# Kernel tuning notes

Hardware: AMD Instinct MI355X
Metric: run time of the kernel (lower is better)

The kernel has to match this reference:

```python
import jax, jax.numpy as jnp
import numpy as np

N_Q = 5000
MEM = 50
KDIM = 50
VDIM = 200
FC = 50
B = 2048
S = 200


def setup_inputs() -> dict:
    key = jax.random.key(0)
    ks = jax.random.split(key, 14)
    inp = {}
    inp["q_data"] = jax.random.randint(ks[0], (B, S), 0, N_Q, dtype=jnp.int64)
    inp["qa_data"] = jax.random.randint(ks[1], (B, S), 0, 2 * N_Q, dtype=jnp.int64)
    # learned parameters (kaiming-ish random init)
    inp["q_embed_w"] = jax.random.normal(ks[2], (N_Q + 1, KDIM), jnp.float32) * 0.2
    inp["qa_embed_w"] = jax.random.normal(ks[3], (2 * N_Q + 1, VDIM), jnp.float32) * 0.1
    inp["key_memory"] = jax.random.normal(ks[4], (MEM, KDIM), jnp.float32) * 0.2
    inp["init_value_memory"] = jax.random.normal(ks[5], (MEM, VDIM), jnp.float32) * 0.1
    # DKVMN write gates: erase (sigmoid) and add (tanh) transforms of qa embedding
    inp["erase_w"] = jax.random.normal(ks[6], (VDIM, VDIM), jnp.float32) * 0.1
    inp["erase_b"] = jnp.zeros((VDIM,), jnp.float32)
    inp["add_w"] = jax.random.normal(ks[7], (VDIM, VDIM), jnp.float32) * 0.1
    inp["add_b"] = jnp.zeros((VDIM,), jnp.float32)
    # prediction MLP: Linear(VDIM+KDIM -> FC), Tanh, Linear(FC -> 1)
    inp["pred_w1"] = jax.random.normal(ks[8], (VDIM + KDIM, FC), jnp.float32) * 0.1
    inp["pred_b1"] = jnp.zeros((FC,), jnp.float32)
    inp["pred_w2"] = jax.random.normal(ks[9], (FC, 1), jnp.float32) * 0.2
    inp["pred_b2"] = jnp.zeros((1,), jnp.float32)
    return inp


def _dkvmn_forward(q_data, qa_data, q_embed_w, qa_embed_w, key_memory,
                   init_value_memory, erase_w, erase_b, add_w, add_b,
                   pred_w1, pred_b1, pred_w2, pred_b2):
    q_emb = q_embed_w[q_data]    # [B, S, KDIM]
    qa_emb = qa_embed_w[qa_data]  # [B, S, VDIM]
    batch = q_data.shape[0]
    Mv0 = jnp.broadcast_to(init_value_memory, (batch, MEM, VDIM))

    def step(Mv, xs):
        q_t, qa_t = xs  # [B, KDIM], [B, VDIM]
        # attention over memory slots
        w = jax.nn.softmax(q_t @ key_memory.T, axis=-1)          # [B, MEM]
        read = jnp.einsum('bm,bmv->bv', w, Mv)                    # [B, VDIM]
        h = jnp.tanh(jnp.concatenate([read, q_t], -1) @ pred_w1 + pred_b1)
        p = jax.nn.sigmoid((h @ pred_w2 + pred_b2)[:, 0])         # [B]
        # erase/add write
        e = jax.nn.sigmoid(qa_t @ erase_w + erase_b)              # [B, VDIM]
        a = jnp.tanh(qa_t @ add_w + add_b)                        # [B, VDIM]
        Mv_new = Mv * (1.0 - w[:, :, None] * e[:, None, :]) + w[:, :, None] * a[:, None, :]
        return Mv_new, p

    xs = (jnp.swapaxes(q_emb, 0, 1), jnp.swapaxes(qa_emb, 0, 1))  # time-major
    _, preds = jax.lax.scan(step, Mv0, xs)                        # [S, B]
    return preds.T                                                # [B, S]


def reference(q_data, qa_data, q_embed_w, qa_embed_w, key_memory,
              init_value_memory, erase_w, erase_b, add_w, add_b,
              pred_w1, pred_b1, pred_w2, pred_b2):
    preds = _dkvmn_forward(q_data, qa_data, q_embed_w, qa_embed_w, key_memory,
                           init_value_memory, erase_w, erase_b, add_w, add_b,
                           pred_w1, pred_b1, pred_w2, pred_b2)
    zeros = jnp.zeros_like(preds)
    return (preds, zeros, zeros, zeros)
```

## Files before the change

kernel.cpp:

```cpp
#include <hip/hip_runtime.h>
#include <hip/hip_fp16.h>


#define NQ1   5001
#define NQA   10001
#define MEMN  50
#define KD    50
#define VD    200
#define FC    50
#define BB    2048
#define SS    200
#define EA_R  16
#define WHS   32

#define EA_B   626
#define WQ_B   1251
#define PACK_B 8
#define PREP_G (EA_B + WQ_B + PACK_B)

typedef unsigned int   u32;
typedef unsigned short u16;
typedef short    s8v __attribute__((ext_vector_type(8)));
typedef float    f4v __attribute__((ext_vector_type(4)));
typedef _Float16 h2v __attribute__((ext_vector_type(2)));
typedef u32      u4v __attribute__((ext_vector_type(4)));

__device__ __forceinline__ float fast_sigmoid(float x) { return 1.f / (1.f + __expf(-x)); }
__device__ __forceinline__ float fast_tanh(float x) {
    float e2 = __expf(2.f * x);
    return 1.f - 2.f / (e2 + 1.f);
}
__device__ __forceinline__ float bfu16_to_f(u16 u) {
    union { float f; u32 i; } x; x.i = ((u32)u) << 16; return x.f;
}
__device__ __forceinline__ u16 f_to_bfu16(float f) {
    union { float f; u32 i; } x; x.f = f;
    return (u16)((x.i + 0x7fffu + ((x.i >> 16) & 1u)) >> 16);
}
__device__ __forceinline__ h2v u32_to_h2v(u32 u) {
    union { u32 i; h2v h; } x; x.i = u; return x.h;
}
__device__ __forceinline__ u16 f16bits(float f) {
    union { __half h; u16 u; } x; x.h = __float2half(f); return x.u;
}
__device__ __forceinline__ float h16_to_f(u16 u) {
    union { u16 u; __half h; } x; x.u = u; return __half2float(x.h);
}

__global__ __launch_bounds__(256) void prep(
        const float* __restrict__ qemb, const float* __restrict__ km,
        const float* __restrict__ w1,   const float* __restrict__ b1,
        const float* __restrict__ qaemb,
        const float* __restrict__ ew,   const float* __restrict__ ebias,
        const float* __restrict__ aw,   const float* __restrict__ abias,
        float* __restrict__ Wt, u32* __restrict__ Wh, float* __restrict__ Q1,
        u32* __restrict__ EA, u16* __restrict__ W1s,
        float* __restrict__ out_aux) {
    const int tid = threadIdx.x;
    const int blk = blockIdx.x;

    for (size_t i = (size_t)blk * 256 + tid; i < 3ull * BB * SS;
         i += (size_t)PREP_G * 256)
        out_aux[i] = 0.f;

    __shared__ float smem[VD * EA_R];

    if (blk < EA_B) {
        const int r0 = blk * EA_R;
        if (tid < VD) {
            #pragma unroll
            for (int r = 0; r < EA_R; ++r) {
                int row = r0 + r;
                smem[tid * EA_R + r] = (row < NQA) ? qaemb[(size_t)row * VD + tid] : 0.f;
            }
        }
        __syncthreads();
        if (tid >= VD) return;

        float accE[EA_R], accA[EA_R];
        #pragma unroll
        for (int r = 0; r < EA_R; ++r) { accE[r] = 0.f; accA[r] = 0.f; }
        for (int k = 0; k < VD; ++k) {
            float we = ew[k * VD + tid];
            float wa = aw[k * VD + tid];
            #pragma unroll
            for (int r = 0; r < EA_R; ++r) {
                float qv = smem[k * EA_R + r];
                accE[r] = fmaf(qv, we, accE[r]);
                accA[r] = fmaf(qv, wa, accA[r]);
            }
        }
        float be = ebias[tid], ba = abias[tid];
        #pragma unroll
        for (int r = 0; r < EA_R; ++r) {
            int row = r0 + r;
            if (row < NQA) {
                u16 ne16 = f16bits(-fast_sigmoid(accE[r] + be));
                u16 a16  = f16bits(fast_tanh(accA[r] + ba));
                EA[(size_t)row * VD + tid] = (u32)ne16 | ((u32)a16 << 16);
            }
        }
    } else if (blk < EA_B + WQ_B) {
        const int lane = tid & 63;
        const int wv   = tid >> 6;
        const int q    = (blk - EA_B) * 4 + wv;
        const bool qok = q < NQ1;
        float* qrow = smem + wv * 64;
        if (qok && lane < KD) qrow[lane] = qemb[q * KD + lane];
        __syncthreads();
        if (!qok) return;

        float s = -1e30f;
        if (lane < MEMN) {
            s = 0.f;
            #pragma unroll
            for (int k = 0; k < KD; ++k) s = fmaf(qrow[k], km[lane * KD + k], s);
        }
        float mx = s;
        #pragma unroll
        for (int off = 32; off >= 1; off >>= 1) mx = fmaxf(mx, __shfl_xor(mx, off, 64));
        float e = (lane < MEMN) ? __expf(s - mx) : 0.f;
        float sum = e;
        #pragma unroll
        for (int off = 32; off >= 1; off >>= 1) sum += __shfl_xor(sum, off, 64);
        float wv_ = (lane < MEMN) ? (e / sum) : 0.f;
        if (lane < MEMN) Wt[q * MEMN + lane] = wv_;

        float plo = __shfl(wv_, 2 * (lane & 31), 64);
        float phi = __shfl(wv_, 2 * (lane & 31) + 1, 64);
        if (lane < 25) {
            Wh[q * WHS + lane] = (u32)f16bits(plo) | ((u32)f16bits(phi) << 16);
        } else if (lane < WHS) {
            Wh[q * WHS + lane] = 0;
        }

        if (lane < FC) {
            float h = b1[lane];
            #pragma unroll
            for (int k = 0; k < KD; ++k)
                h = fmaf(qrow[k], w1[(VD + k) * FC + lane], h);
            Q1[q * FC + lane] = h;
        }
    } else {
        for (int idx = (blk - EA_B - WQ_B) * 256 + tid; idx < 4 * 7 * 64 * 8;
             idx += PACK_B * 256) {
            int j    = idx & 7;
            int lane = (idx >> 3) & 63;
            int kt   = (idx >> 9) % 7;
            int nt   = idx / 3584;
            int k = kt * 32 + ((lane >> 4) << 3) + j;
            int n = nt * 16 + (lane & 15);
            float v = (k < VD && n < FC) ? w1[k * FC + n] : 0.f;
            W1s[idx] = f_to_bfu16(v);
        }
    }
}

__device__ __forceinline__ void state_step(const u32 (&w)[25], u32 ea,
                                           h2v (&mv)[25], float& rdA, float& rdB) {
    h2v nev2 = u32_to_h2v(__builtin_amdgcn_perm(ea, ea, 0x01000100u));
    h2v av2  = u32_to_h2v(__builtin_amdgcn_perm(ea, ea, 0x03020302u));
    rdA = 0.f; rdB = 0.f;
    #pragma unroll
    for (int i = 0; i < 25; i += 2) {
        h2v w0 = u32_to_h2v(w[i]);
#if __has_builtin(__builtin_amdgcn_fdot2)
        rdA = __builtin_amdgcn_fdot2(w0, mv[i], rdA, false);
#else
        rdA = fmaf((float)w0.x, (float)mv[i].x,
              fmaf((float)w0.y, (float)mv[i].y, rdA));
#endif
        mv[i] = __builtin_elementwise_fma(
            w0, __builtin_elementwise_fma(nev2, mv[i], av2), mv[i]);
        if (i + 1 < 25) {
            h2v w1p = u32_to_h2v(w[i + 1]);
#if __has_builtin(__builtin_amdgcn_fdot2)
            rdB = __builtin_amdgcn_fdot2(w1p, mv[i + 1], rdB, false);
#else
            rdB = fmaf((float)w1p.x, (float)mv[i + 1].x,
                  fmaf((float)w1p.y, (float)mv[i + 1].y, rdB));
#endif
            mv[i + 1] = __builtin_elementwise_fma(
                w1p, __builtin_elementwise_fma(nev2, mv[i + 1], av2), mv[i + 1]);
        }
    }
}

__global__ __launch_bounds__(128) void dkvmn_state(
        const int* __restrict__ qd, const int* __restrict__ qad,
        const u32* __restrict__ Wh, const u32* __restrict__ EA,
        const float* __restrict__ ivm, u16* __restrict__ READ) {
    const int tid  = threadIdx.x;
    const int lane = tid & 63;
    const int wid  = tid >> 6;
    const int blk  = blockIdx.x;
    const int b    = blk >> 1;
    const int role = (blk & 1) * 2 + wid;
    const int base = b * SS;

    if (role < 3) {
        const int v = role * 64 + lane;

        h2v mv[25];
        #pragma unroll
        for (int i = 0; i < 25; ++i) {
            mv[i].x = (_Float16)ivm[(2 * i) * VD + v];
            mv[i].y = (_Float16)ivm[(2 * i + 1) * VD + v];
        }

        int q_c = __builtin_amdgcn_readfirstlane(qd[base]);
        int q_n = __builtin_amdgcn_readfirstlane(qd[base + 1]);
        int qa0 = __builtin_amdgcn_readfirstlane(qad[base]);
        int qa1 = __builtin_amdgcn_readfirstlane(qad[base + 1]);
        u32 ea_c = EA[(size_t)qa0 * VD + v];
        u32 ea_n = EA[(size_t)qa1 * VD + v];

        u32 wb0[25], wb1[25];
        #pragma unroll
        for (int i = 0; i < 25; ++i) wb0[i] = Wh[(size_t)q_c * WHS + i];

        for (int t = 0; t < SS; t += 2) {
            {
                #pragma unroll
                for (int i = 0; i < 25; ++i) wb1[i] = Wh[(size_t)q_n * WHS + i];

                int tn = t + 2; tn = (tn < SS) ? tn : (SS - 1);
                int q_nn  = __builtin_amdgcn_readfirstlane(qd[base + tn]);
                int qa_nn = __builtin_amdgcn_readfirstlane(qad[base + tn]);
                u32 ea_nn = EA[(size_t)qa_nn * VD + v];

                float rdA, rdB;
                state_step(wb0, ea_c, mv, rdA, rdB);
                READ[(size_t)(base + t) * VD + v] = f_to_bfu16(rdA + rdB);
                q_c = q_n; q_n = q_nn; ea_c = ea_n; ea_n = ea_nn;
            }
            {
                #pragma unroll
                for (int i = 0; i < 25; ++i) wb0[i] = Wh[(size_t)q_n * WHS + i];

                int tn = t + 3; tn = (tn < SS) ? tn : (SS - 1);
                int q_nn  = __builtin_amdgcn_readfirstlane(qd[base + tn]);
                int qa_nn = __builtin_amdgcn_readfirstlane(qad[base + tn]);
                u32 ea_nn = EA[(size_t)qa_nn * VD + v];

                float rdA, rdB;
                state_step(wb1, ea_c, mv, rdA, rdB);
                READ[(size_t)(base + t + 1) * VD + v] = f_to_bfu16(rdA + rdB);
                q_c = q_n; q_n = q_nn; ea_c = ea_n; ea_n = ea_nn;
            }
        }
    } else {
        const int v8  = lane & 7;
        const int grp = lane >> 3;
        const int v   = 192 + v8;

        h2v mv4[4];
        #pragma unroll
        for (int j = 0; j < 4; ++j) {
            int p = grp * 4 + j;
            if (p < 25) {
                mv4[j].x = (_Float16)ivm[(2 * p) * VD + v];
                mv4[j].y = (_Float16)ivm[(2 * p + 1) * VD + v];
            } else {
                mv4[j].x = (_Float16)0.f;
                mv4[j].y = (_Float16)0.f;
            }
        }

        int q_c = __builtin_amdgcn_readfirstlane(qd[base]);
        int q_n = __builtin_amdgcn_readfirstlane(qd[base + 1]);
        int qa0 = __builtin_amdgcn_readfirstlane(qad[base]);
        int qa1 = __builtin_amdgcn_readfirstlane(qad[base + 1]);
        u32 ea_c = EA[(size_t)qa0 * VD + v];
        u32 ea_n = EA[(size_t)qa1 * VD + v];
        u4v wq_c = *(const u4v*)(Wh + (size_t)q_c * WHS + grp * 4);
        u4v wq_n = *(const u4v*)(Wh + (size_t)q_n * WHS + grp * 4);

        for (int t = 0; t < SS; ++t) {
            int tn = t + 2; tn = (tn < SS) ? tn : (SS - 1);
            int q_nn  = __builtin_amdgcn_readfirstlane(qd[base + tn]);
            int qa_nn = __builtin_amdgcn_readfirstlane(qad[base + tn]);
            u32 ea_nn = EA[(size_t)qa_nn * VD + v];
            u4v wq_nn = *(const u4v*)(Wh + (size_t)q_nn * WHS + grp * 4);

            h2v nev2 = u32_to_h2v(__builtin_amdgcn_perm(ea_c, ea_c, 0x01000100u));
            h2v av2  = u32_to_h2v(__builtin_amdgcn_perm(ea_c, ea_c, 0x03020302u));

            float rd = 0.f;
            #pragma unroll
            for (int j = 0; j < 4; ++j) {
                h2v w2 = u32_to_h2v(wq_c[j]);
#if __has_builtin(__builtin_amdgcn_fdot2)
                rd = __builtin_amdgcn_fdot2(w2, mv4[j], rd, false);
#else
                rd = fmaf((float)w2.x, (float)mv4[j].x,
                     fmaf((float)w2.y, (float)mv4[j].y, rd));
#endif
                mv4[j] = __builtin_elementwise_fma(
                    w2, __builtin_elementwise_fma(nev2, mv4[j], av2), mv4[j]);
            }
            rd += __shfl_xor(rd, 8, 64);
            rd += __shfl_xor(rd, 16, 64);
            rd += __shfl_xor(rd, 32, 64);
            if (grp == 0)
                READ[(size_t)(base + t) * VD + v] = f_to_bfu16(rd);

            q_c = q_n; q_n = q_nn; ea_c = ea_n; ea_n = ea_nn;
            wq_c = wq_n; wq_n = wq_nn;
        }
    }
}

__global__ __launch_bounds__(256) void mlp_pred(
        const u16* __restrict__ RD, const int* __restrict__ qd,
        const float* __restrict__ Q1tab, const u16* __restrict__ W1s,
        const float* __restrict__ w2, const float* __restrict__ b2,
        float* __restrict__ out) {
    const int tid  = threadIdx.x;
    const int lane = tid & 63;
    const int wv   = tid >> 6;
    const int strip = blockIdx.x * 4 + wv;
    const int row0  = strip * 16;

    const int mrow = lane & 15;
    const int quad = lane >> 4;

    s8v a[7];
    {
        const u16* arow = RD + (size_t)(row0 + mrow) * VD + quad * 8;
        #pragma unroll
        for (int kt = 0; kt < 7; ++kt)
            a[kt] = *(const s8v*)(arow + kt * 32);
    }

    const float b2f = b2[0];
    float pf[4] = {0.f, 0.f, 0.f, 0.f};

    #pragma unroll
    for (int nt = 0; nt < 4; ++nt) {
        s8v bfr[7];
        #pragma unroll
        for (int kt = 0; kt < 7; ++kt)
            bfr[kt] = *(const s8v*)(W1s + (((nt * 7 + kt) * 64) + lane) * 8);

        f4v acc = {0.f, 0.f, 0.f, 0.f};
        #pragma unroll
        for (int kt = 0; kt < 7; ++kt)
            acc = __builtin_amdgcn_mfma_f32_16x16x32_bf16(a[kt], bfr[kt], acc, 0, 0, 0);

        const int f = nt * 16 + mrow;
        const float w2f = (f < FC) ? w2[f] : 0.f;
        #pragma unroll
        for (int r = 0; r < 4; ++r) {
            int row = row0 + quad * 4 + r;
            float h = acc[r] + Q1tab[qd[row] * FC + f];
            pf[r] = fmaf(fast_tanh(h), w2f, pf[r]);
        }
    }

    #pragma unroll
    for (int r = 0; r < 4; ++r) {
        float s = pf[r];
        s += __shfl_xor(s, 1, 64);
        s += __shfl_xor(s, 2, 64);
        s += __shfl_xor(s, 4, 64);
        s += __shfl_xor(s, 8, 64);
        if (mrow == 0)
            out[row0 + quad * 4 + r] = fast_sigmoid(s + b2f);
    }
}

__global__ void dkvmn_main(const int* __restrict__ qd, const int* __restrict__ qad,
                           const float* __restrict__ Wtab, const float* __restrict__ Q1tab,
                           const u32* __restrict__ EA,
                           const float* __restrict__ ivm,
                           const float* __restrict__ w1,
                           const float* __restrict__ w2,
                           const float* __restrict__ b2,
                           float* __restrict__ out) {
    const int tid  = threadIdx.x;
    const int b    = blockIdx.x;
    const int v    = tid;
    const int lane = tid & 63;
    const int wv   = tid >> 6;

    __shared__ alignas(16) float read_lds[4 * 52];
    __shared__ alignas(16) float part_lds[4 * 52];

    float mv[MEMN];
    if (v < VD) {
        #pragma unroll
        for (int m = 0; m < MEMN; ++m) mv[m] = ivm[m * VD + v];
    }
    float w1r[50];
    if (lane < FC) {
        #pragma unroll
        for (int i = 0; i < 50; ++i) w1r[i] = w1[(wv * 50 + i) * FC + lane];
    } else {
        #pragma unroll
        for (int i = 0; i < 50; ++i) w1r[i] = 0.f;
    }
    const float w2f = (tid < FC) ? w2[tid] : 0.f;
    const float b2f = b2[0];

    const int* qrow_i  = qd  + b * SS;
    const int* qarow_i = qad + b * SS;
    const int jchunk = v / 50;
    const int wslot  = jchunk * 52 + (v - jchunk * 50);

    for (int t = 0; t < SS; ++t) {
        const int q  = __builtin_amdgcn_readfirstlane(qrow_i[t]);
        const int qa = __builtin_amdgcn_readfirstlane(qarow_i[t]);
        const float* wrow = Wtab + q * MEMN;

        u32 ea = 0;
        if (v < VD) ea = EA[(size_t)qa * VD + v];
        float ne = h16_to_f((u16)(ea & 0xffffu));
        float av = h16_to_f((u16)(ea >> 16));

        if (v < VD) {
            float rd0 = 0.f, rd1 = 0.f;
            #pragma unroll
            for (int m = 0; m < MEMN; m += 2) {
                float wm0 = wrow[m], wm1 = wrow[m + 1];
                rd0 = fmaf(wm0, mv[m], rd0);
                mv[m] = fmaf(wm0, fmaf(ne, mv[m], av), mv[m]);
                rd1 = fmaf(wm1, mv[m + 1], rd1);
                mv[m + 1] = fmaf(wm1, fmaf(ne, mv[m + 1], av), mv[m + 1]);
            }
            read_lds[wslot] = rd0 + rd1;
        }
        __syncthreads();

        float part = 0.f;
        {
            const float* rlc = read_lds + wv * 52;
            #pragma unroll
            for (int i = 0; i < 48; i += 4) {
                float4 x = *(const float4*)(rlc + i);
                part = fmaf(x.x, w1r[i],     part);
                part = fmaf(x.y, w1r[i + 1], part);
                part = fmaf(x.z, w1r[i + 2], part);
                part = fmaf(x.w, w1r[i + 3], part);
            }
            part = fmaf(rlc[48], w1r[48], part);
            part = fmaf(rlc[49], w1r[49], part);
        }
        if (lane < FC) part_lds[wv * 52 + lane] = part;
        __syncthreads();

        if (wv == 0) {
            float pf = 0.f;
            if (lane < FC) {
                float h = part_lds[lane] + part_lds[52 + lane] +
                          part_lds[104 + lane] + part_lds[156 + lane] +
                          Q1tab[q * FC + lane];
                pf = fast_tanh(h) * w2f;
            }
            #pragma unroll
            for (int off = 32; off >= 1; off >>= 1) pf += __shfl_xor(pf, off, 64);
            if (lane == 0) out[b * SS + t] = fast_sigmoid(pf + b2f);
        }
    }
}

extern "C" void kernel_launch(void* const* d_in, const int* in_sizes, int n_in,
                              void* d_out, int out_size, void* d_ws, size_t ws_size,
                              hipStream_t stream) {
    const int* qd  = (const int*)d_in[0];
    const int* qad = (const int*)d_in[1];
    const float* qemb  = (const float*)d_in[2];
    const float* qaemb = (const float*)d_in[3];
    const float* km    = (const float*)d_in[4];
    const float* ivm   = (const float*)d_in[5];
    const float* ew    = (const float*)d_in[6];
    const float* eb    = (const float*)d_in[7];
    const float* aw    = (const float*)d_in[8];
    const float* ab    = (const float*)d_in[9];
    const float* w1    = (const float*)d_in[10];
    const float* b1    = (const float*)d_in[11];
    const float* w2    = (const float*)d_in[12];
    const float* b2    = (const float*)d_in[13];
    float* out = (float*)d_out;
    (void)in_sizes; (void)n_in; (void)out_size;

    char* ws = (char*)d_ws;
    float* Wt  = (float*)(ws);
    float* Q1  = (float*)(ws + 1000448);
    u32*   EA  = (u32*)  (ws + 2000896);
    u16*   W1s = (u16*)  (ws + 10001920);
    u32*   Wh  = (u32*)  (ws + 10034688);
    u16*   RD  = (u16*)  (ws + 10675200);
    const size_t need = 10675200ull + 163840000ull + 512ull;

    prep<<<PREP_G, 256, 0, stream>>>(qemb, km, w1, b1, qaemb, ew, eb, aw, ab,
                                     Wt, Wh, Q1, EA, W1s, out + (size_t)BB * SS);

    if (ws_size >= need) {
        dkvmn_state<<<BB * 2, 128, 0, stream>>>(qd, qad, Wh, EA, ivm, RD);
        mlp_pred<<<(BB * SS) / 64, 256, 0, stream>>>(RD, qd, Q1, W1s, w2, b2, out);
    } else {
        dkvmn_main<<<BB, 256, 0, stream>>>(qd, qad, Wt, Q1, EA, ivm, w1, w2, b2, out);
    }
}
```

Measured before the change: 434.0 us.

## Stage question indices in LDS and load Wh rows as vector VGPR loads

The per-sequence q and qa indices are copied once into shared memory, so each step reads them from LDS instead of issuing scalar global loads. The 25-word attention row is now fetched with six 16-byte vector loads plus one word per lane, where before it was 25 uniform scalar loads. The loop is no longer manually unrolled into two halves with a double-buffered register array. Instead it prefetches indices three steps ahead and the next Wh row one step ahead. This is meant to cut scalar-memory latency and register pressure in the serial recurrence, at the cost of per-lane vector loads of uniform data and an LDS fill with a block barrier.

```diff
diff --git a/kernel.cpp b/kernel.cpp
--- a/kernel.cpp
+++ b/kernel.cpp
@@ -156,14 +156,15 @@
     }
 }
 
-__device__ __forceinline__ void state_step(const u32 (&w)[25], u32 ea,
-                                           h2v (&mv)[25], float& rdA, float& rdB) {
+__device__ __forceinline__ void state_step_v(const u4v (&w)[6], u32 w6, u32 ea,
+                                             h2v (&mv)[25], float& rdA, float& rdB) {
     h2v nev2 = u32_to_h2v(__builtin_amdgcn_perm(ea, ea, 0x01000100u));
     h2v av2  = u32_to_h2v(__builtin_amdgcn_perm(ea, ea, 0x03020302u));
     rdA = 0.f; rdB = 0.f;
     #pragma unroll
     for (int i = 0; i < 25; i += 2) {
-        h2v w0 = u32_to_h2v(w[i]);
+        u32 wu0 = (i < 24) ? w[i >> 2][i & 3] : w6;
+        h2v w0 = u32_to_h2v(wu0);
 #if __has_builtin(__builtin_amdgcn_fdot2)
         rdA = __builtin_amdgcn_fdot2(w0, mv[i], rdA, false);
 #else
@@ -173,7 +174,7 @@
         mv[i] = __builtin_elementwise_fma(
             w0, __builtin_elementwise_fma(nev2, mv[i], av2), mv[i]);
         if (i + 1 < 25) {
-            h2v w1p = u32_to_h2v(w[i + 1]);
+            h2v w1p = u32_to_h2v(w[(i + 1) >> 2][(i + 1) & 3]);
 #if __has_builtin(__builtin_amdgcn_fdot2)
             rdB = __builtin_amdgcn_fdot2(w1p, mv[i + 1], rdB, false);
 #else
@@ -198,6 +199,13 @@
     const int role = (blk & 1) * 2 + wid;
     const int base = b * SS;
 
+    __shared__ int qs[SS], qas[SS];
+    for (int i = tid; i < SS; i += 128) {
+        qs[i]  = qd[base + i];
+        qas[i] = qad[base + i];
+    }
+    __syncthreads();
+
     if (role < 3) {
         const int v = role * 64 + lane;
 
@@ -208,46 +216,41 @@
             mv[i].y = (_Float16)ivm[(2 * i + 1) * VD + v];
         }
 
-        int q_c = __builtin_amdgcn_readfirstlane(qd[base]);
-        int q_n = __builtin_amdgcn_readfirstlane(qd[base + 1]);
-        int qa0 = __builtin_amdgcn_readfirstlane(qad[base]);
-        int qa1 = __builtin_amdgcn_readfirstlane(qad[base + 1]);
-        u32 ea_c = EA[(size_t)qa0 * VD + v];
-        u32 ea_n = EA[(size_t)qa1 * VD + v];
-
-        u32 wb0[25], wb1[25];
-        #pragma unroll
-        for (int i = 0; i < 25; ++i) wb0[i] = Wh[(size_t)q_c * WHS + i];
-
-        for (int t = 0; t < SS; t += 2) {
+        int q0  = qs[0];  asm volatile("" : "+v"(q0));
+        int qw  = qs[1];  asm volatile("" : "+v"(qw));
+        int qw2 = qs[2];  asm volatile("" : "+v"(qw2));
+        int qa2 = qas[2];
+        u32 ea_c = EA[(size_t)qas[0] * VD + v];
+        u32 ea_n = EA[(size_t)qas[1] * VD + v];
+
+        u4v wA[6]; u32 wA6;
+        {
+            const u32* rp = Wh + (size_t)q0 * WHS;
+            #pragma unroll
+            for (int j = 0; j < 6; ++j) wA[j] = *(const u4v*)(rp + j * 4);
+            wA6 = rp[24];
+        }
+
+        for (int t = 0; t < SS; ++t) {
+            int t3 = t + 3; t3 = (t3 < SS) ? t3 : (SS - 1);
+            int qnew  = qs[t3];  asm volatile("" : "+v"(qnew));
+            int qanew = qas[t3];
+
+            u32 ea_f = EA[(size_t)qa2 * VD + v];
+
+            float rdA, rdB;
+            state_step_v(wA, wA6, ea_c, mv, rdA, rdB);
+            READ[(size_t)(base + t) * VD + v] = f_to_bfu16(rdA + rdB);
+
             {
+                const u32* rp = Wh + (size_t)qw * WHS;
                 #pragma unroll
-                for (int i = 0; i < 25; ++i) wb1[i] = Wh[(size_t)q_n * WHS + i];
-
-                int tn = t + 2; tn = (tn < SS) ? tn : (SS - 1);
-                int q_nn  = __builtin_amdgcn_readfirstlane(qd[base + tn]);
-                int qa_nn = __builtin_amdgcn_readfirstlane(qad[base + tn]);
-                u32 ea_nn = EA[(size_t)qa_nn * VD + v];
-
-                float rdA, rdB;
-                state_step(wb0, ea_c, mv, rdA, rdB);
-                READ[(size_t)(base + t) * VD + v] = f_to_bfu16(rdA + rdB);
-                q_c = q_n; q_n = q_nn; ea_c = ea_n; ea_n = ea_nn;
-            }
-            {
-                #pragma unroll
-                for (int i = 0; i < 25; ++i) wb0[i] = Wh[(size_t)q_n * WHS + i];
-
-                int tn = t + 3; tn = (tn < SS) ? tn : (SS - 1);
-                int q_nn  = __builtin_amdgcn_readfirstlane(qd[base + tn]);
-                int qa_nn = __builtin_amdgcn_readfirstlane(qad[base + tn]);
-                u32 ea_nn = EA[(size_t)qa_nn * VD + v];
-
-                float rdA, rdB;
-                state_step(wb1, ea_c, mv, rdA, rdB);
-                READ[(size_t)(base + t + 1) * VD + v] = f_to_bfu16(rdA + rdB);
-                q_c = q_n; q_n = q_nn; ea_c = ea_n; ea_n = ea_nn;
-            }
+                for (int j = 0; j < 6; ++j) wA[j] = *(const u4v*)(rp + j * 4);
+                wA6 = rp[24];
+            }
+
+            qw = qw2; qw2 = qnew; qa2 = qanew;
+            ea_c = ea_n; ea_n = ea_f;
         }
     } else {
         const int v8  = lane & 7;
@@ -267,19 +270,16 @@
             }
         }
 
-        int q_c = __builtin_amdgcn_readfirstlane(qd[base]);
-        int q_n = __builtin_amdgcn_readfirstlane(qd[base + 1]);
-        int qa0 = __builtin_amdgcn_readfirstlane(qad[base]);
-        int qa1 = __builtin_amdgcn_readfirstlane(qad[base + 1]);
-        u32 ea_c = EA[(size_t)qa0 * VD + v];
-        u32 ea_n = EA[(size_t)qa1 * VD + v];
-        u4v wq_c = *(const u4v*)(Wh + (size_t)q_c * WHS + grp * 4);
-        u4v wq_n = *(const u4v*)(Wh + (size_t)q_n * WHS + grp * 4);
+        int q0 = qs[0], q1 = qs[1];
+        u32 ea_c = EA[(size_t)qas[0] * VD + v];
+        u32 ea_n = EA[(size_t)qas[1] * VD + v];
+        u4v wq_c = *(const u4v*)(Wh + (size_t)q0 * WHS + grp * 4);
+        u4v wq_n = *(const u4v*)(Wh + (size_t)q1 * WHS + grp * 4);
 
         for (int t = 0; t < SS; ++t) {
             int tn = t + 2; tn = (tn < SS) ? tn : (SS - 1);
-            int q_nn  = __builtin_amdgcn_readfirstlane(qd[base + tn]);
-            int qa_nn = __builtin_amdgcn_readfirstlane(qad[base + tn]);
+            int q_nn  = qs[tn];
+            int qa_nn = qas[tn];
             u32 ea_nn = EA[(size_t)qa_nn * VD + v];
             u4v wq_nn = *(const u4v*)(Wh + (size_t)q_nn * WHS + grp * 4);
 
@@ -305,7 +305,7 @@
             if (grp == 0)
                 READ[(size_t)(base + t) * VD + v] = f_to_bfu16(rd);
 
-            q_c = q_n; q_n = q_nn; ea_c = ea_n; ea_n = ea_nn;
+            ea_c = ea_n; ea_n = ea_nn;
             wq_c = wq_n; wq_n = wq_nn;
         }
     }
```

After: 507.3 us. +16.9%, slower.
